# Kernel tuning notes

Measured on AMD Instinct MI355X. Metric: run time of the kernel, lower is better.

## Reference

```python
import jax, jax.numpy as jnp
import numpy as np

V, E, H, L, S, B, FE = 50257, 768, 12, 4, 1024, 2, 4
HD = E // H
EPS = 1e-5


def setup_inputs() -> dict:
    key = jax.random.key(0)
    ks = jax.random.split(key, 16)
    def n(k, shape, scale=0.02):
        return jax.random.normal(k, shape, jnp.float32) * scale
    x = jax.random.randint(ks[0], (B, S), 0, V)
    mask = jnp.tril(jnp.ones((S, S), jnp.int32))[None, None]  # (1,1,S,S) causal
    return {
        "x": x,
        "mask": mask,
        "embed_W": n(ks[1], (V, E)),
        "pos_embed": n(ks[2], (1, S, E)),
        "fc_out_W": n(ks[3], (L, E, E)),
        "fc_out_b": jnp.zeros((L, E), jnp.float32),
        "gate_W": n(ks[4], (L, E, E)),
        "gate_b": jnp.zeros((L, E), jnp.float32),
        "ln1_g": jnp.ones((L, E), jnp.float32),
        "ln1_b": jnp.zeros((L, E), jnp.float32),
        "ln2_g": jnp.ones((L, E), jnp.float32),
        "ln2_b": jnp.zeros((L, E), jnp.float32),
        "ff1_W": n(ks[5], (L, E, FE * E)),
        "ff1_b": jnp.zeros((L, FE * E), jnp.float32),
        "ff2_W": n(ks[6], (L, FE * E, E)),
        "ff2_b": jnp.zeros((L, E), jnp.float32),
        "lnf_g": jnp.ones((E,), jnp.float32),
        "lnf_b": jnp.zeros((E,), jnp.float32),
        "head_W": n(ks[7], (E, V)),
    }


def _layernorm(y, g, b):
    m = jnp.mean(y, -1, keepdims=True)
    v = jnp.mean((y - m) ** 2, -1, keepdims=True)
    return (y - m) * jax.lax.rsqrt(v + EPS) * g + b


def reference(x, mask, embed_W, pos_embed, fc_out_W, fc_out_b, gate_W, gate_b,
              ln1_g, ln1_b, ln2_g, ln2_b, ff1_W, ff1_b, ff2_W, ff2_b,
              lnf_g, lnf_b, head_W):
    h = embed_W[x] + pos_embed[:, :x.shape[1], :]  # (B,S,E)
    scale = 1.0 / np.sqrt(HD)
    for i in range(L):
        # NOTE: source never applies the q/k/v Linear layers; heads are split directly.
        q = h.reshape(B, S, H, HD).transpose(0, 2, 1, 3)  # (B,H,S,HD)
        energy = jnp.einsum('bhqd,bhkd->bhqk', q, q)
        energy = jnp.where(mask == 0, jnp.float32(-1e20), energy)
        attn = jax.nn.softmax(energy * scale, axis=-1)
        o = jnp.einsum('bhqk,bhkd->bhqd', attn, q)
        o = o.transpose(0, 2, 1, 3).reshape(B, S, E)
        o = o @ fc_out_W[i] + fc_out_b[i]
        gate = jax.nn.sigmoid(jnp.mean(h, 1, keepdims=True) @ gate_W[i] + gate_b[i])
        h = _layernorm(gate * o + h, ln1_g[i], ln1_b[i])
        ff = jax.nn.gelu(h @ ff1_W[i] + ff1_b[i], approximate=False) @ ff2_W[i] + ff2_b[i]
        h = _layernorm(ff + h, ln2_g[i], ln2_b[i])
    h = _layernorm(h, lnf_g, lnf_b)
    logits = h @ head_W  # (B,S,V)
    return logits
```

## Files before the change

kernel.cpp:

```cpp
#include <hip/hip_runtime.h>
#include <hip/hip_bf16.h>

#define V 50257
#define E 768
#define NH 12
#define NL 4
#define SS 1024
#define BB 2
#define FEE 4
#define HD 64
#define EPSL 1e-5f
#define NPADH 50432

typedef __hip_bfloat16 bf16;
typedef __attribute__((ext_vector_type(8))) short short8;
typedef __attribute__((ext_vector_type(4))) float f32x4;

#define GLD_SRC(p) (const __attribute__((address_space(1))) void*)(p)
#define GLD_DST(p) (__attribute__((address_space(3))) void*)(p)

__global__ __launch_bounds__(256) void embed_kernel(const int* __restrict__ x, const float* __restrict__ eW,
                                                    const float* __restrict__ pos, float* __restrict__ h){
  size_t i = (size_t)blockIdx.x*256 + threadIdx.x;
  if (i >= (size_t)BB*SS*E) return;
  int e = (int)(i % E);
  size_t bs = i / E;
  int s = (int)(bs % SS);
  int tok = x[bs];
  h[i] = eW[(size_t)tok*E + e] + pos[(size_t)s*E + e];
}

__global__ __launch_bounds__(256) void cvt_attn(const float* __restrict__ h, bf16* __restrict__ hb,
                                                bf16* __restrict__ vT){
  __shared__ float t[64][65];
  int bid = blockIdx.x;
  int st = bid & 15, hh = (bid >> 4) % NH, b = bid / (16*NH);
  int s0 = st*64;
  int c = threadIdx.x & 63, rr = threadIdx.x >> 6;
  #pragma unroll
  for (int i = 0; i < 16; ++i){
    int r = rr*16 + i;
    float v = h[(size_t)(b*SS + s0 + r)*E + hh*HD + c];
    hb[(size_t)(b*SS + s0 + r)*E + hh*HD + c] = __float2bfloat16(v);
    t[r][c] = v;
  }
  __syncthreads();
  #pragma unroll
  for (int i = 0; i < 16; ++i){
    int d = rr*16 + i;
    vT[(size_t)((b*NH + hh)*HD + d)*SS + s0 + c] = __float2bfloat16(t[c][d]);
  }
}

__global__ __launch_bounds__(256) void attn_mfma(const bf16* __restrict__ hb, const bf16* __restrict__ vT,
                                                 bf16* __restrict__ Ab){
  __shared__ short Qs[64*64];
  __shared__ short Ks[128*64];
  __shared__ short Vs[64*128];
  __shared__ short Ps[4][16*128];
  int tid = threadIdx.x, wave = tid >> 6, lane = tid & 63;
  int bid = blockIdx.x;
  int qt = 15 - (bid & 15);
  int hh = (bid >> 4) % NH, b = bid / (16*NH);
  int q0 = qt*64;
  int l15 = lane & 15, l4 = lane >> 4;
  int sw7 = l15 & 7;

  #pragma unroll
  for (int rnd = 0; rnd < 2; ++rnd){
    int o = rnd*256 + tid; int row = o >> 3; int cs = (((o & 7) ^ (row & 7))*8);
    __builtin_amdgcn_global_load_lds(GLD_SRC(hb + ((size_t)(b*SS + q0 + row)*E + hh*HD + cs)),
                                     GLD_DST(Qs + o*8), 16, 0, 0);
  }

  float mrun[4], lrun[4];
  #pragma unroll
  for (int j = 0; j < 4; ++j){ mrun[j] = -1e30f; lrun[j] = 0.f; }
  f32x4 acco[4] = {};

  int nkt = (qt >> 1) + 1;
  for (int kt = 0; kt < nkt; ++kt){
    int k0 = kt*128;
    __syncthreads();
    #pragma unroll
    for (int rnd = 0; rnd < 4; ++rnd){
      int o = rnd*256 + tid; int row = o >> 3; int cs = (((o & 7) ^ (row & 7))*8);
      __builtin_amdgcn_global_load_lds(GLD_SRC(hb + ((size_t)(b*SS + k0 + row)*E + hh*HD + cs)),
                                       GLD_DST(Ks + o*8), 16, 0, 0);
    }
    #pragma unroll
    for (int rnd = 0; rnd < 4; ++rnd){
      int o = rnd*256 + tid; int row = o >> 4; int cs = (((o & 15) ^ (row & 15))*8);
      __builtin_amdgcn_global_load_lds(GLD_SRC(vT + ((size_t)((b*NH + hh)*HD + row)*SS + k0 + cs)),
                                       GLD_DST(Vs + o*8), 16, 0, 0);
    }
    __syncthreads();

    f32x4 s[8] = {};
    __builtin_amdgcn_s_setprio(1);
    #pragma unroll
    for (int kk = 0; kk < 2; ++kk){
      int slot = kk*4 + l4;
      short8 af = *(const short8*)&Qs[(wave*16 + l15)*64 + ((slot ^ sw7)*8)];
      #pragma unroll
      for (int n = 0; n < 8; ++n){
        short8 bf8 = *(const short8*)&Ks[(n*16 + l15)*64 + ((slot ^ sw7)*8)];
        s[n] = __builtin_amdgcn_mfma_f32_16x16x32_bf16(af, bf8, s[n], 0, 0, 0);
      }
    }
    __builtin_amdgcn_s_setprio(0);

    bool diag = (kt == nkt - 1);
    #pragma unroll
    for (int j = 0; j < 4; ++j){
      int qg = q0 + wave*16 + l4*4 + j;
      float tmax = -1e30f;
      #pragma unroll
      for (int n = 0; n < 8; ++n){
        float v = s[n][j]*0.125f;
        if (diag && (k0 + n*16 + l15) > qg) v = -1e30f;
        s[n][j] = v; tmax = fmaxf(tmax, v);
      }
      tmax = fmaxf(tmax, __shfl_xor(tmax, 1, 64));
      tmax = fmaxf(tmax, __shfl_xor(tmax, 2, 64));
      tmax = fmaxf(tmax, __shfl_xor(tmax, 4, 64));
      tmax = fmaxf(tmax, __shfl_xor(tmax, 8, 64));
      float mnew = fmaxf(mrun[j], tmax);
      float alpha = __expf(mrun[j] - mnew);
      float rsum = 0.f;
      #pragma unroll
      for (int n = 0; n < 8; ++n){
        float p = __expf(s[n][j] - mnew);
        s[n][j] = p; rsum += p;
      }
      rsum += __shfl_xor(rsum, 1, 64);
      rsum += __shfl_xor(rsum, 2, 64);
      rsum += __shfl_xor(rsum, 4, 64);
      rsum += __shfl_xor(rsum, 8, 64);
      lrun[j] = lrun[j]*alpha + rsum;
      mrun[j] = mnew;
      #pragma unroll
      for (int n = 0; n < 4; ++n) acco[n][j] *= alpha;
      int prow = l4*4 + j;
      #pragma unroll
      for (int n = 0; n < 8; ++n){
        bf16 hv = __float2bfloat16(s[n][j]);
        int slot = (n*2 + (l15 >> 3)) ^ prow;
        Ps[wave][prow*128 + slot*8 + (l15 & 7)] = __builtin_bit_cast(short, hv);
      }
    }
    __syncthreads();

    __builtin_amdgcn_s_setprio(1);
    #pragma unroll
    for (int kk = 0; kk < 4; ++kk){
      int slot = kk*4 + l4;
      short8 pa = *(const short8*)&Ps[wave][l15*128 + ((slot ^ l15)*8)];
      #pragma unroll
      for (int n = 0; n < 4; ++n){
        short8 vb = *(const short8*)&Vs[(n*16 + l15)*128 + ((slot ^ l15)*8)];
        acco[n] = __builtin_amdgcn_mfma_f32_16x16x32_bf16(pa, vb, acco[n], 0, 0, 0);
      }
    }
    __builtin_amdgcn_s_setprio(0);
  }

  #pragma unroll
  for (int j = 0; j < 4; ++j){
    float inv = 1.f / lrun[j];
    int qg = q0 + wave*16 + l4*4 + j;
    #pragma unroll
    for (int n = 0; n < 4; ++n){
      Ab[(size_t)(b*SS + qg)*E + hh*HD + n*16 + l15] = __float2bfloat16(acco[n][j]*inv);
    }
  }
}

__global__ __launch_bounds__(256) void hmean1_kernel(const float* __restrict__ h, float* __restrict__ ph){
  int bid = blockIdx.x;
  int ec = bid % 3, tc = (bid/3) & 15, b = bid / 48;
  int e = ec*256 + threadIdx.x;
  float s = 0.f;
  #pragma unroll 8
  for (int t = tc*64; t < tc*64 + 64; ++t) s += h[((size_t)b*SS + t)*E + e];
  ph[((size_t)b*16 + tc)*E + e] = s;
}
__global__ __launch_bounds__(256) void hmean2_kernel(const float* __restrict__ ph, float* __restrict__ hm){
  int idx = blockIdx.x*256 + threadIdx.x;
  if (idx >= BB*E) return;
  int b = idx / E, e = idx % E;
  float s = 0.f;
  #pragma unroll
  for (int tc = 0; tc < 16; ++tc) s += ph[((size_t)b*16 + tc)*E + e];
  hm[idx] = s * (1.0f/SS);
}

__global__ __launch_bounds__(256) void gate1_kernel(const float* __restrict__ hm, const float* __restrict__ gW,
                                                    float* __restrict__ pg){
  int bid = blockIdx.x;
  int ec = bid % 3, kc = (bid/3) & 3, b = bid / 12;
  int nn = ec*256 + threadIdx.x;
  float acc = 0.f;
  #pragma unroll 8
  for (int k = kc*192; k < kc*192 + 192; ++k) acc += hm[b*E + k] * gW[(size_t)k*E + nn];
  pg[((size_t)b*4 + kc)*E + nn] = acc;
}
__global__ __launch_bounds__(256) void gate2_kernel(const float* __restrict__ pg, const float* __restrict__ gb,
                                                    float* __restrict__ gv){
  int idx = blockIdx.x*256 + threadIdx.x;
  if (idx >= BB*E) return;
  int b = idx / E, nn = idx % E;
  float acc = pg[(size_t)(b*4+0)*E + nn] + pg[(size_t)(b*4+1)*E + nn]
            + pg[(size_t)(b*4+2)*E + nn] + pg[(size_t)(b*4+3)*E + nn] + gb[nn];
  gv[idx] = 1.0f / (1.0f + __expf(-acc));
}

__global__ __launch_bounds__(256) void wcvt_kernel(const float* __restrict__ W, bf16* __restrict__ Wt,
                                                   int K, int N, int Npad){
  int l = blockIdx.z;
  W  += (size_t)l*K*N;
  Wt += (size_t)l*Npad*K;
  __shared__ float t[32][33];
  int n0 = blockIdx.x*32, k0 = blockIdx.y*32;
  int tx = threadIdx.x & 31, ty8 = threadIdx.x >> 5;
  #pragma unroll
  for (int i = 0; i < 4; ++i){
    int k = k0 + ty8 + i*8, n = n0 + tx;
    t[ty8 + i*8][tx] = (k < K && n < N) ? W[(size_t)k*N + n] : 0.f;
  }
  __syncthreads();
  #pragma unroll
  for (int i = 0; i < 4; ++i){
    int n = n0 + ty8 + i*8, k = k0 + tx;
    if (n < Npad && k < K) Wt[(size_t)n*K + k] = __float2bfloat16(t[tx][ty8 + i*8]);
  }
}

template<int EPI>
__global__ __launch_bounds__(256) void mfma_gemm(const bf16* __restrict__ A, const bf16* __restrict__ Bt,
                                                 const float* __restrict__ bias, void* __restrict__ Cv,
                                                 int M, int N, int K){
  __shared__ short As[128*64];
  __shared__ short Bs[128*64];
  int tid = threadIdx.x;
  int wave = tid >> 6, lane = tid & 63;
  int wr = wave >> 1, wc = wave & 1;
  int l15 = lane & 15, l4 = lane >> 4;
  int sw7 = l15 & 7;
  int n0 = blockIdx.x * 128, m0 = blockIdx.y * 128;
  f32x4 acc[4][4] = {};
  int srow = tid >> 3;
  int sj = tid & 7;
  const int nks = K >> 6;
  for (int kt = 0; kt < nks; ++kt){
    int kbase = kt * 64;
    __syncthreads();
    #pragma unroll
    for (int iss = 0; iss < 4; ++iss){
      int r = srow + iss*32;
      int cs = ((sj ^ (r & 7))*8);
      __builtin_amdgcn_global_load_lds(GLD_SRC(A + (size_t)(m0 + r)*K + kbase + cs),
                                       GLD_DST(As + r*64 + sj*8), 16, 0, 0);
      __builtin_amdgcn_global_load_lds(GLD_SRC(Bt + (size_t)(n0 + r)*K + kbase + cs),
                                       GLD_DST(Bs + r*64 + sj*8), 16, 0, 0);
    }
    __syncthreads();
    #pragma unroll
    for (int kk = 0; kk < 2; ++kk){
      int slot = kk*4 + l4;
      short8 af[4], bfr[4];
      #pragma unroll
      for (int m = 0; m < 4; ++m)
        af[m] = *(const short8*)&As[(wr*64 + m*16 + l15)*64 + ((slot ^ sw7)*8)];
      #pragma unroll
      for (int n = 0; n < 4; ++n)
        bfr[n] = *(const short8*)&Bs[(wc*64 + n*16 + l15)*64 + ((slot ^ sw7)*8)];
      #pragma unroll
      for (int m = 0; m < 4; ++m)
        #pragma unroll
        for (int n = 0; n < 4; ++n)
          acc[m][n] = __builtin_amdgcn_mfma_f32_16x16x32_bf16(af[m], bfr[n], acc[m][n], 0, 0, 0);
    }
  }
  int lrow = l4*4;
  #pragma unroll
  for (int m = 0; m < 4; ++m){
    int row = m0 + wr*64 + m*16 + lrow;
    #pragma unroll
    for (int n = 0; n < 4; ++n){
      int col = n0 + wc*64 + n*16 + l15;
      if (col >= N) continue;
      float bv = bias[col];
      #pragma unroll
      for (int j = 0; j < 4; ++j){
        float v = acc[m][n][j] + bv;
        if (EPI == 3){
          v = 0.5f*v*(1.0f + erff(v*0.70710678f));
          ((bf16*)Cv)[(size_t)(row + j)*N + col] = __float2bfloat16(v);
        } else {
          ((float*)Cv)[(size_t)(row + j)*N + col] = v;
        }
      }
    }
  }
}

__global__ __launch_bounds__(512, 2) void gemm256(const bf16* __restrict__ A, const bf16* __restrict__ Bt,
                                                  float* __restrict__ C, int M, int N, int K, int MT){
  __shared__ short As[2][256*64];
  __shared__ short Bs[2][256*64];
  int tid = threadIdx.x;
  int wave = tid >> 6, lane = tid & 63;
  int wr = wave >> 2, wc = wave & 3;
  int l15 = lane & 15, l4 = lane >> 4;
  int sw7 = l15 & 7;

  int lid = blockIdx.x;
  int cpx = gridDim.x >> 3;
  int wg = (lid & 7)*cpx + (lid >> 3);
  int m0 = (wg % MT)*256, n0 = (wg / MT)*256;

  int srow = tid >> 3;
  int sj = tid & 7;
  const int nks = K >> 6;

  #define STAGE256(bsel, kt) do {                                             \
    int kb = (kt)*64;                                                         \
    _Pragma("unroll")                                                         \
    for (int rnd = 0; rnd < 4; ++rnd){                                        \
      int r = rnd*64 + srow;                                                  \
      int cs = ((sj ^ (r & 7))*8);                                            \
      __builtin_amdgcn_global_load_lds(GLD_SRC(A + (size_t)(m0 + r)*K + kb + cs),   \
                                       GLD_DST(&As[bsel][r*64 + sj*8]), 16, 0, 0);  \
      __builtin_amdgcn_global_load_lds(GLD_SRC(Bt + (size_t)(n0 + r)*K + kb + cs),  \
                                       GLD_DST(&Bs[bsel][r*64 + sj*8]), 16, 0, 0);  \
    }                                                                         \
  } while(0)

  f32x4 acc[8][4] = {};
  STAGE256(0, 0);
  for (int kt = 0; kt < nks; ++kt){
    int cur = kt & 1;
    __syncthreads();
    if (kt + 1 < nks) STAGE256(cur ^ 1, kt + 1);
    __builtin_amdgcn_s_setprio(1);
    #pragma unroll
    for (int kk = 0; kk < 2; ++kk){
      int slot = kk*4 + l4;
      short8 af[8], bfr[4];
      #pragma unroll
      for (int m = 0; m < 8; ++m)
        af[m] = *(const short8*)&As[cur][(wr*128 + m*16 + l15)*64 + ((slot ^ sw7)*8)];
      #pragma unroll
      for (int n = 0; n < 4; ++n)
        bfr[n] = *(const short8*)&Bs[cur][(wc*64 + n*16 + l15)*64 + ((slot ^ sw7)*8)];
      #pragma unroll
      for (int m = 0; m < 8; ++m)
        #pragma unroll
        for (int n = 0; n < 4; ++n)
          acc[m][n] = __builtin_amdgcn_mfma_f32_16x16x32_bf16(af[m], bfr[n], acc[m][n], 0, 0, 0);
    }
    __builtin_amdgcn_s_setprio(0);
  }
  #undef STAGE256

  int lrow = l4*4;
  #pragma unroll
  for (int m = 0; m < 8; ++m){
    int row = m0 + wr*128 + m*16 + lrow;
    #pragma unroll
    for (int n = 0; n < 4; ++n){
      int col = n0 + wc*64 + n*16 + l15;
      if (col >= N) continue;
      #pragma unroll
      for (int j = 0; j < 4; ++j)
        C[(size_t)(row + j)*N + col] = acc[m][n][j];
    }
  }
}

__global__ __launch_bounds__(256) void ln_kernel(const float* __restrict__ a, const float* __restrict__ resid,
                                                 const float* __restrict__ gatev, const float* __restrict__ g,
                                                 const float* __restrict__ bta, float* __restrict__ out,
                                                 bf16* __restrict__ outb){
  int row = blockIdx.x;
  int b = row >> 10;
  int tid = threadIdx.x;
  __shared__ float sred[4];
  float y[3];
  float lsum = 0.f;
  #pragma unroll
  for (int i = 0; i < 3; ++i){
    int e = tid + i*256;
    float v = a[(size_t)row*E + e];
    if (gatev) v *= gatev[b*E + e];
    if (resid) v += resid[(size_t)row*E + e];
    y[i] = v; lsum += v;
  }
  for (int off = 32; off > 0; off >>= 1) lsum += __shfl_down(lsum, off, 64);
  int wid = tid >> 6, lane = tid & 63;
  if (lane == 0) sred[wid] = lsum;
  __syncthreads();
  float mean = (sred[0]+sred[1]+sred[2]+sred[3]) * (1.0f/E);
  __syncthreads();
  float lvar = 0.f;
  #pragma unroll
  for (int i = 0; i < 3; ++i){ float d = y[i]-mean; lvar += d*d; }
  for (int off = 32; off > 0; off >>= 1) lvar += __shfl_down(lvar, off, 64);
  if (lane == 0) sred[wid] = lvar;
  __syncthreads();
  float rstd = rsqrtf((sred[0]+sred[1]+sred[2]+sred[3]) * (1.0f/E) + EPSL);
  __syncthreads();
  #pragma unroll
  for (int i = 0; i < 3; ++i){
    int e = tid + i*256;
    float r = (y[i]-mean)*rstd*g[e] + bta[e];
    out[(size_t)row*E + e] = r;
    if (outb) outb[(size_t)row*E + e] = __float2bfloat16(r);
  }
}

extern "C" void kernel_launch(void* const* d_in, const int* in_sizes, int n_in,
                              void* d_out, int out_size, void* d_ws, size_t ws_size,
                              hipStream_t stream) {
  const int*   x      = (const int*)  d_in[0];
  const float* embedW = (const float*)d_in[2];
  const float* pos    = (const float*)d_in[3];
  const float* fcW    = (const float*)d_in[4];
  const float* fcB    = (const float*)d_in[5];
  const float* gW     = (const float*)d_in[6];
  const float* gB     = (const float*)d_in[7];
  const float* ln1g   = (const float*)d_in[8];
  const float* ln1b   = (const float*)d_in[9];
  const float* ln2g   = (const float*)d_in[10];
  const float* ln2b   = (const float*)d_in[11];
  const float* f1W    = (const float*)d_in[12];
  const float* f1B    = (const float*)d_in[13];
  const float* f2W    = (const float*)d_in[14];
  const float* f2B    = (const float*)d_in[15];
  const float* lnfg   = (const float*)d_in[16];
  const float* lnfb   = (const float*)d_in[17];
  const float* headW  = (const float*)d_in[18];
  float* out = (float*)d_out;

  const size_t BSE = (size_t)BB*SS*E;
  float* h    = (float*)d_ws;
  float* o    = h   + BSE;
  float* tmp  = o   + BSE;
  float* hm   = tmp + BSE;
  float* gv   = hm  + (size_t)BB*E;
  float* ph   = gv  + (size_t)BB*E;
  float* pg   = ph  + (size_t)BB*16*E;
  bf16* abA   = (bf16*)(pg + (size_t)BB*4*E);
  bf16* abF   = abA + BSE;
  bf16* WfcT  = abF + BSE*FEE;
  bf16* Wf1T  = WfcT + (size_t)NL*E*E;
  bf16* Wf2T  = Wf1T + (size_t)NL*FEE*E*E;
  bf16* WheadT= Wf2T + (size_t)NL*FEE*E*E;
  bf16* hb    = (bf16*)o;
  bf16* vT    = hb + BSE;

  const int rows = BB*SS;

  embed_kernel<<<(int)((BSE + 255)/256), 256, 0, stream>>>(x, embedW, pos, h);

  { dim3 g(E/32, E/32, NL);        wcvt_kernel<<<g, 256, 0, stream>>>(fcW, WfcT, E, E, E); }
  { dim3 g((FEE*E)/32, E/32, NL);  wcvt_kernel<<<g, 256, 0, stream>>>(f1W, Wf1T, E, FEE*E, FEE*E); }
  { dim3 g(E/32, (FEE*E)/32, NL);  wcvt_kernel<<<g, 256, 0, stream>>>(f2W, Wf2T, FEE*E, E, E); }
  { dim3 g(NPADH/32, E/32, 1);     wcvt_kernel<<<g, 256, 0, stream>>>(headW, WheadT, E, V, NPADH); }

  for (int l = 0; l < NL; ++l){
    size_t oEE = (size_t)l*E*E, oE = (size_t)l*E, oFb = (size_t)l*FEE*E;

    hmean1_kernel<<<BB*16*3, 256, 0, stream>>>(h, ph);
    hmean2_kernel<<<(BB*E + 255)/256, 256, 0, stream>>>(ph, hm);
    gate1_kernel<<<BB*4*3, 256, 0, stream>>>(hm, gW + oEE, pg);
    gate2_kernel<<<(BB*E + 255)/256, 256, 0, stream>>>(pg, gB + oE, gv);

    cvt_attn<<<BB*NH*16, 256, 0, stream>>>(h, hb, vT);
    attn_mfma<<<BB*NH*16, 256, 0, stream>>>(hb, vT, abA);

    { dim3 g(E/128, rows/128);
      mfma_gemm<0><<<g, 256, 0, stream>>>(abA, WfcT + oEE, fcB + oE, tmp, rows, E, E); }

    ln_kernel<<<rows, 256, 0, stream>>>(tmp, h, gv, ln1g + oE, ln1b + oE, h, abA);

    { dim3 g((FEE*E)/128, rows/128);
      mfma_gemm<3><<<g, 256, 0, stream>>>(abA, Wf1T + (size_t)l*FEE*E*E, f1B + oFb, abF, rows, FEE*E, E); }

    { dim3 g(E/128, rows/128);
      mfma_gemm<0><<<g, 256, 0, stream>>>(abF, Wf2T + (size_t)l*FEE*E*E, f2B + oE, tmp, rows, E, FEE*E); }

    ln_kernel<<<rows, 256, 0, stream>>>(tmp, h, nullptr, ln2g + oE, ln2b + oE, h, nullptr);
  }

  ln_kernel<<<rows, 256, 0, stream>>>(h, nullptr, nullptr, lnfg, lnfb, tmp, abA);
  {
    gemm256<<<(rows/256)*(NPADH/256), 512, 0, stream>>>(abA, WheadT, out, rows, V, E, rows/256);
  }
}
```

Before: 1.201 ms.

## Double-buffer GEMM, split-K the narrow GEMMs, fold gate/mean into neighbors

The 128x128 MFMA GEMM now double-buffers its LDS tiles so the next K-tile loads while the current one computes, and it raises wave priority around the MFMA block. The two N=768 GEMMs (fc_out and ff2) are split along K into two slices to raise the block count, and the partial sums plus bias are reduced inside the layernorm kernel. The hmean2 and gate2 kernels are removed: the mean finalization moves into gate1, and the sigmoid gate is computed inside ln_kernel. The cost is extra partial-sum traffic through a second full-size fp32 buffer, twice the LDS per block, and the sigmoid being recomputed for every row.

```diff
diff --git a/kernel.cpp b/kernel.cpp
--- a/kernel.cpp
+++ b/kernel.cpp
@@ -185,34 +185,25 @@
   for (int t = tc*64; t < tc*64 + 64; ++t) s += h[((size_t)b*SS + t)*E + e];
   ph[((size_t)b*16 + tc)*E + e] = s;
 }
-__global__ __launch_bounds__(256) void hmean2_kernel(const float* __restrict__ ph, float* __restrict__ hm){
-  int idx = blockIdx.x*256 + threadIdx.x;
-  if (idx >= BB*E) return;
-  int b = idx / E, e = idx % E;
-  float s = 0.f;
-  #pragma unroll
-  for (int tc = 0; tc < 16; ++tc) s += ph[((size_t)b*16 + tc)*E + e];
-  hm[idx] = s * (1.0f/SS);
-}
-
-__global__ __launch_bounds__(256) void gate1_kernel(const float* __restrict__ hm, const float* __restrict__ gW,
+
+__global__ __launch_bounds__(256) void gate1_kernel(const float* __restrict__ ph, const float* __restrict__ gW,
                                                     float* __restrict__ pg){
   int bid = blockIdx.x;
   int ec = bid % 3, kc = (bid/3) & 3, b = bid / 12;
   int nn = ec*256 + threadIdx.x;
+  __shared__ float hms[192];
+  if (threadIdx.x < 192){
+    int k = kc*192 + threadIdx.x;
+    float s = 0.f;
+    #pragma unroll
+    for (int tc = 0; tc < 16; ++tc) s += ph[((size_t)b*16 + tc)*E + k];
+    hms[threadIdx.x] = s * (1.0f/SS);
+  }
+  __syncthreads();
   float acc = 0.f;
   #pragma unroll 8
-  for (int k = kc*192; k < kc*192 + 192; ++k) acc += hm[b*E + k] * gW[(size_t)k*E + nn];
+  for (int j = 0; j < 192; ++j) acc += hms[j] * gW[(size_t)(kc*192 + j)*E + nn];
   pg[((size_t)b*4 + kc)*E + nn] = acc;
-}
-__global__ __launch_bounds__(256) void gate2_kernel(const float* __restrict__ pg, const float* __restrict__ gb,
-                                                    float* __restrict__ gv){
-  int idx = blockIdx.x*256 + threadIdx.x;
-  if (idx >= BB*E) return;
-  int b = idx / E, nn = idx % E;
-  float acc = pg[(size_t)(b*4+0)*E + nn] + pg[(size_t)(b*4+1)*E + nn]
-            + pg[(size_t)(b*4+2)*E + nn] + pg[(size_t)(b*4+3)*E + nn] + gb[nn];
-  gv[idx] = 1.0f / (1.0f + __expf(-acc));
 }
 
 __global__ __launch_bounds__(256) void wcvt_kernel(const float* __restrict__ W, bf16* __restrict__ Wt,
@@ -239,49 +230,62 @@
 template<int EPI>
 __global__ __launch_bounds__(256) void mfma_gemm(const bf16* __restrict__ A, const bf16* __restrict__ Bt,
                                                  const float* __restrict__ bias, void* __restrict__ Cv,
-                                                 int M, int N, int K){
-  __shared__ short As[128*64];
-  __shared__ short Bs[128*64];
+                                                 int M, int N, int Kslice, int Ktot){
+  __shared__ short As[2][128*64];
+  __shared__ short Bs[2][128*64];
   int tid = threadIdx.x;
   int wave = tid >> 6, lane = tid & 63;
   int wr = wave >> 1, wc = wave & 1;
   int l15 = lane & 15, l4 = lane >> 4;
   int sw7 = l15 & 7;
   int n0 = blockIdx.x * 128, m0 = blockIdx.y * 128;
+  size_t koff = (size_t)blockIdx.z * Kslice;
   f32x4 acc[4][4] = {};
   int srow = tid >> 3;
   int sj = tid & 7;
-  const int nks = K >> 6;
+  const int nks = Kslice >> 6;
+
+  #define STAGE128(bsel, kt) do {                                              \
+    int kb = (kt)*64;                                                          \
+    _Pragma("unroll")                                                          \
+    for (int iss = 0; iss < 4; ++iss){                                         \
+      int r = srow + iss*32;                                                   \
+      int cs = ((sj ^ (r & 7))*8);                                             \
+      __builtin_amdgcn_global_load_lds(GLD_SRC(A + (size_t)(m0 + r)*Ktot + koff + kb + cs),  \
+                                       GLD_DST(&As[bsel][r*64 + sj*8]), 16, 0, 0);           \
+      __builtin_amdgcn_global_load_lds(GLD_SRC(Bt + (size_t)(n0 + r)*Ktot + koff + kb + cs), \
+                                       GLD_DST(&Bs[bsel][r*64 + sj*8]), 16, 0, 0);           \
+    }                                                                          \
+  } while(0)
+
+  STAGE128(0, 0);
+  __syncthreads();
   for (int kt = 0; kt < nks; ++kt){
-    int kbase = kt * 64;
-    __syncthreads();
-    #pragma unroll
-    for (int iss = 0; iss < 4; ++iss){
-      int r = srow + iss*32;
-      int cs = ((sj ^ (r & 7))*8);
-      __builtin_amdgcn_global_load_lds(GLD_SRC(A + (size_t)(m0 + r)*K + kbase + cs),
-                                       GLD_DST(As + r*64 + sj*8), 16, 0, 0);
-      __builtin_amdgcn_global_load_lds(GLD_SRC(Bt + (size_t)(n0 + r)*K + kbase + cs),
-                                       GLD_DST(Bs + r*64 + sj*8), 16, 0, 0);
-    }
-    __syncthreads();
+    int cur = kt & 1;
+    if (kt + 1 < nks) STAGE128(cur ^ 1, kt + 1);
+    __builtin_amdgcn_s_setprio(1);
     #pragma unroll
     for (int kk = 0; kk < 2; ++kk){
       int slot = kk*4 + l4;
       short8 af[4], bfr[4];
       #pragma unroll
       for (int m = 0; m < 4; ++m)
-        af[m] = *(const short8*)&As[(wr*64 + m*16 + l15)*64 + ((slot ^ sw7)*8)];
+        af[m] = *(const short8*)&As[cur][(wr*64 + m*16 + l15)*64 + ((slot ^ sw7)*8)];
       #pragma unroll
       for (int n = 0; n < 4; ++n)
-        bfr[n] = *(const short8*)&Bs[(wc*64 + n*16 + l15)*64 + ((slot ^ sw7)*8)];
+        bfr[n] = *(const short8*)&Bs[cur][(wc*64 + n*16 + l15)*64 + ((slot ^ sw7)*8)];
       #pragma unroll
       for (int m = 0; m < 4; ++m)
         #pragma unroll
         for (int n = 0; n < 4; ++n)
           acc[m][n] = __builtin_amdgcn_mfma_f32_16x16x32_bf16(af[m], bfr[n], acc[m][n], 0, 0, 0);
     }
-  }
+    __builtin_amdgcn_s_setprio(0);
+    __syncthreads();
+  }
+  #undef STAGE128
+
+  float* Cf = (float*)Cv + (size_t)blockIdx.z * M * N;
   int lrow = l4*4;
   #pragma unroll
   for (int m = 0; m < 4; ++m){
@@ -290,15 +294,15 @@
     for (int n = 0; n < 4; ++n){
       int col = n0 + wc*64 + n*16 + l15;
       if (col >= N) continue;
-      float bv = bias[col];
       #pragma unroll
       for (int j = 0; j < 4; ++j){
-        float v = acc[m][n][j] + bv;
+        float v = acc[m][n][j];
         if (EPI == 3){
+          v += bias[col];
           v = 0.5f*v*(1.0f + erff(v*0.70710678f));
           ((bf16*)Cv)[(size_t)(row + j)*N + col] = __float2bfloat16(v);
         } else {
-          ((float*)Cv)[(size_t)(row + j)*N + col] = v;
+          Cf[(size_t)(row + j)*N + col] = v;
         }
       }
     }
@@ -339,9 +343,9 @@
 
   f32x4 acc[8][4] = {};
   STAGE256(0, 0);
+  __syncthreads();
   for (int kt = 0; kt < nks; ++kt){
     int cur = kt & 1;
-    __syncthreads();
     if (kt + 1 < nks) STAGE256(cur ^ 1, kt + 1);
     __builtin_amdgcn_s_setprio(1);
     #pragma unroll
@@ -361,6 +365,7 @@
           acc[m][n] = __builtin_amdgcn_mfma_f32_16x16x32_bf16(af[m], bfr[n], acc[m][n], 0, 0, 0);
     }
     __builtin_amdgcn_s_setprio(0);
+    __syncthreads();
   }
   #undef STAGE256
 
@@ -379,10 +384,13 @@
   }
 }
 
-__global__ __launch_bounds__(256) void ln_kernel(const float* __restrict__ a, const float* __restrict__ resid,
-                                                 const float* __restrict__ gatev, const float* __restrict__ g,
-                                                 const float* __restrict__ bta, float* __restrict__ out,
-                                                 bf16* __restrict__ outb){
+__global__ __launch_bounds__(256) void ln_kernel(const float* __restrict__ parts, int np,
+                                                 const float* __restrict__ bias,
+                                                 const float* __restrict__ resid,
+                                                 const float* __restrict__ pg, const float* __restrict__ gb,
+                                                 const float* __restrict__ g, const float* __restrict__ bta,
+                                                 float* __restrict__ out, bf16* __restrict__ outb){
+  const size_t PS = (size_t)BB*SS*E;
   int row = blockIdx.x;
   int b = row >> 10;
   int tid = threadIdx.x;
@@ -392,8 +400,13 @@
   #pragma unroll
   for (int i = 0; i < 3; ++i){
     int e = tid + i*256;
-    float v = a[(size_t)row*E + e];
-    if (gatev) v *= gatev[b*E + e];
+    float v = bias ? bias[e] : 0.f;
+    for (int p = 0; p < np; ++p) v += parts[(size_t)p*PS + (size_t)row*E + e];
+    if (pg){
+      float ga = pg[(size_t)(b*4+0)*E + e] + pg[(size_t)(b*4+1)*E + e]
+               + pg[(size_t)(b*4+2)*E + e] + pg[(size_t)(b*4+3)*E + e] + gb[e];
+      v *= 1.0f / (1.0f + __expf(-ga));
+    }
     if (resid) v += resid[(size_t)row*E + e];
     y[i] = v; lsum += v;
   }
@@ -447,9 +460,7 @@
   float* h    = (float*)d_ws;
   float* o    = h   + BSE;
   float* tmp  = o   + BSE;
-  float* hm   = tmp + BSE;
-  float* gv   = hm  + (size_t)BB*E;
-  float* ph   = gv  + (size_t)BB*E;
+  float* ph   = tmp + 2*BSE;
   float* pg   = ph  + (size_t)BB*16*E;
   bf16* abA   = (bf16*)(pg + (size_t)BB*4*E);
   bf16* abF   = abA + BSE;
@@ -473,28 +484,29 @@
     size_t oEE = (size_t)l*E*E, oE = (size_t)l*E, oFb = (size_t)l*FEE*E;
 
     hmean1_kernel<<<BB*16*3, 256, 0, stream>>>(h, ph);
-    hmean2_kernel<<<(BB*E + 255)/256, 256, 0, stream>>>(ph, hm);
-    gate1_kernel<<<BB*4*3, 256, 0, stream>>>(hm, gW + oEE, pg);
-    gate2_kernel<<<(BB*E + 255)/256, 256, 0, stream>>>(pg, gB + oE, gv);
+    gate1_kernel<<<BB*4*3, 256, 0, stream>>>(ph, gW + oEE, pg);
 
     cvt_attn<<<BB*NH*16, 256, 0, stream>>>(h, hb, vT);
     attn_mfma<<<BB*NH*16, 256, 0, stream>>>(hb, vT, abA);
 
-    { dim3 g(E/128, rows/128);
-      mfma_gemm<0><<<g, 256, 0, stream>>>(abA, WfcT + oEE, fcB + oE, tmp, rows, E, E); }
-
-    ln_kernel<<<rows, 256, 0, stream>>>(tmp, h, gv, ln1g + oE, ln1b + oE, h, abA);
-
-    { dim3 g((FEE*E)/128, rows/128);
-      mfma_gemm<3><<<g, 256, 0, stream>>>(abA, Wf1T + (size_t)l*FEE*E*E, f1B + oFb, abF, rows, FEE*E, E); }
-
-    { dim3 g(E/128, rows/128);
-      mfma_gemm<0><<<g, 256, 0, stream>>>(abF, Wf2T + (size_t)l*FEE*E*E, f2B + oE, tmp, rows, E, FEE*E); }
-
-    ln_kernel<<<rows, 256, 0, stream>>>(tmp, h, nullptr, ln2g + oE, ln2b + oE, h, nullptr);
-  }
-
-  ln_kernel<<<rows, 256, 0, stream>>>(h, nullptr, nullptr, lnfg, lnfb, tmp, abA);
+    { dim3 g(E/128, rows/128, 2);
+      mfma_gemm<0><<<g, 256, 0, stream>>>(abA, WfcT + oEE, nullptr, tmp, rows, E, E/2, E); }
+
+    ln_kernel<<<rows, 256, 0, stream>>>(tmp, 2, fcB + oE, h, pg, gB + oE,
+                                        ln1g + oE, ln1b + oE, h, abA);
+
+    { dim3 g((FEE*E)/128, rows/128, 1);
+      mfma_gemm<3><<<g, 256, 0, stream>>>(abA, Wf1T + (size_t)l*FEE*E*E, f1B + oFb, abF, rows, FEE*E, E, E); }
+
+    { dim3 g(E/128, rows/128, 2);
+      mfma_gemm<0><<<g, 256, 0, stream>>>(abF, Wf2T + (size_t)l*FEE*E*E, nullptr, tmp, rows, E, FEE*E/2, FEE*E); }
+
+    ln_kernel<<<rows, 256, 0, stream>>>(tmp, 2, f2B + oE, h, nullptr, nullptr,
+                                        ln2g + oE, ln2b + oE, h, nullptr);
+  }
+
+  ln_kernel<<<rows, 256, 0, stream>>>(h, 1, nullptr, nullptr, nullptr, nullptr,
+                                      lnfg, lnfb, tmp, abA);
   {
     gemm256<<<(rows/256)*(NPADH/256), 512, 0, stream>>>(abA, WheadT, out, rows, V, E, rows/256);
   }
```

New measurement: 1.030 ms. 1.17x faster.
